# Kernel tuning notes

Measured on AMD Instinct MI355X. Metric: run time of the kernel, lower is better.

The kernel has to match this reference:

```python
import jax, jax.numpy as jnp
import numpy as np

# H36M parent-child joint pairs (the second assignment in the source overrides the first)
PARENT = np.array([[0,1],[1,2],[2,3],[0,4],[4,5],[5,6],[0,8],[8,14],[14,15],[15,16],[8,11],[11,12],[12,13],[8,10]])
NUM_JOINTS = 17
NUM_PAIRS = 14
GRID = 64


def create_heatmap(joint2d, size):
    # Gaussian with cov = 2*I evaluated on integer grid, normalized by its max.
    # Original: grid[i, j] = N([i, j]; mean=[x, y], 2I) / max -> pdf constant cancels.
    xy = joint2d * 64.0  # (B, J, 2)
    ii = jnp.arange(size, dtype=joint2d.dtype)
    dx = ii[None, None, :, None] - xy[..., 0][..., None, None]  # (B, J, size, 1)
    dy = ii[None, None, None, :] - xy[..., 1][..., None, None]  # (B, J, 1, size)
    d2 = dx * dx + dy * dy  # (B, J, size, size)
    g = jnp.exp(-d2 / 4.0)  # exp(-d2 / (2*var)), var = 2
    return g / jnp.max(g, axis=(2, 3), keepdims=True)


def setup_inputs() -> dict:
    key = jax.random.key(0)
    k1, k2, k3, k4 = jax.random.split(key, 4)
    B = 256
    return {
        "pred": jax.random.normal(k1, (B, NUM_JOINTS, 3), dtype=jnp.float32),
        "joints": jax.random.normal(k2, (B, NUM_JOINTS, 3), dtype=jnp.float32),
        "middle_out": jax.random.normal(k3, (B, NUM_JOINTS + 3 * NUM_PAIRS, GRID, GRID), dtype=jnp.float32),
        "joint2d": jax.random.uniform(k4, (B, NUM_JOINTS, 2), dtype=jnp.float32),
    }


def reference(pred, joints, middle_out, joint2d):
    eps = 0.1
    B, _, H, W = middle_out.shape
    # l3D: joints last dim == 3 branch
    l3d = jnp.mean(jnp.sum(jnp.abs(joints - pred[:, :NUM_JOINTS, :]), axis=(1, 2)))

    heatmap = create_heatmap(joint2d, H)  # (B, 17, 64, 64)

    # L2D: mean over batch of sum over joints of squared Frobenius norm (detached in original)
    diff = middle_out[:, :NUM_JOINTS] - heatmap
    L2D = jnp.mean(jnp.sum(jnp.sum(diff * diff, axis=(2, 3)), axis=1))

    # LHEM: vectorized heatmap triplets over batch and all 14 parent/child pairs
    p_idx = PARENT[:, 0]
    c_idx = PARENT[:, 1]
    hp = heatmap[:, p_idx]  # (B, 14, 64, 64)
    hc = heatmap[:, c_idx]  # (B, 14, 64, 64)
    d = joints[:, p_idx, 2] - joints[:, c_idx, 2]  # (B, 14)
    r = jnp.where(d > eps, 1, jnp.where(jnp.abs(d) < eps, 0, -1))[..., None, None]
    ch0 = jnp.where(r == -1, hc, 0.0)
    ch1 = jnp.where(r == 0, hp + hc, hp)
    ch2 = jnp.where(r == 1, hc, 0.0)
    T_GT = jnp.stack((ch0, ch1, ch2), axis=2)  # (B, 14, 3, 64, 64)
    T_pred = middle_out[:, NUM_JOINTS:NUM_JOINTS + 3 * NUM_PAIRS].reshape(B, NUM_PAIRS, 3, H, W)
    norms = jnp.sqrt(jnp.sum((T_GT - T_pred) ** 2, axis=(3, 4)))  # (B, 14, 3)
    LHEM = jnp.mean(jnp.sum(jnp.sum(norms, axis=2) ** 2, axis=1))

    Lint = 0.005 * (LHEM + L2D)
    # Original computes L2D / LHEM in detached numpy -> no gradient through Lint
    return l3d + jax.lax.stop_gradient(Lint)
```

## Files before the change

### kernel.cpp

```cpp
#include <hip/hip_runtime.h>
#include <math.h>

#define NJ 17
#define NP 14
#define NCH 59
#define BATCH 256
#define PSTRIDE 64

__constant__ int c_par0[NP] = {0, 1, 2, 0, 4, 5, 0, 8, 14, 15, 8, 11, 12, 8};
__constant__ int c_par1[NP] = {1, 2, 3, 4, 5, 6, 8, 14, 15, 16, 11, 12, 13, 10};

__device__ __forceinline__ float wave_reduce(float v) {
    #pragma unroll
    for (int off = 32; off; off >>= 1) v += __shfl_down(v, off, 64);
    return v;
}

__device__ __forceinline__ void heat_params(const float* __restrict__ joint2d,
                                            int b, int j,
                                            float& x, float& y, float& m) {
    x = joint2d[(b * NJ + j) * 2 + 0] * 64.f;
    y = joint2d[(b * NJ + j) * 2 + 1] * 64.f;
    const float rx = fminf(fmaxf(floorf(x + 0.5f), 0.f), 63.f);
    const float ry = fminf(fmaxf(floorf(y + 0.5f), 0.f), 63.f);
    m = (rx - x) * (rx - x) + (ry - y) * (ry - y);
}

__global__ __launch_bounds__(256) void slice_sum_kernel(
    const float* __restrict__ pred,
    const float* __restrict__ joints,
    const float* __restrict__ middle,
    const float* __restrict__ joint2d,
    float* __restrict__ partial)
{
    const int c   = blockIdx.x;
    const int b   = blockIdx.y;
    const int tid = threadIdx.x;

    const float4* __restrict__ src =
        (const float4*)(middle + ((size_t)b * NCH + c) * 4096);
    float4 r0 = src[tid];
    float4 r1 = src[tid + 256];
    float4 r2 = src[tid + 512];
    float4 r3 = src[tid + 768];

    float wp = 0.f, wc = 0.f;
    int jp = 0, jc = 0;
    if (c < NJ) {
        jp = c; wp = 1.f;
    } else {
        const int pi = c - NJ;
        const int p  = pi / 3;
        const int ch = pi - p * 3;
        jp = c_par0[p];
        jc = c_par1[p];
        const float dz = joints[(b * NJ + jp) * 3 + 2] - joints[(b * NJ + jc) * 3 + 2];
        const int rsign = (dz > 0.1f) ? 1 : ((fabsf(dz) < 0.1f) ? 0 : -1);
        if (ch == 0)      { wp = 0.f; wc = (rsign == -1) ? 1.f : 0.f; }
        else if (ch == 1) { wp = 1.f; wc = (rsign ==  0) ? 1.f : 0.f; }
        else              { wp = 0.f; wc = (rsign ==  1) ? 1.f : 0.f; }
    }

    float xp = 0.f, yp = 0.f, mp = 0.f;
    float xq = 0.f, yq = 0.f, mq = 0.f;
    if (wp != 0.f) heat_params(joint2d, b, jp, xp, yp, mp);
    if (wc != 0.f) heat_params(joint2d, b, jc, xq, yq, mq);

    const float col0 = (float)((4 * tid) & 63);
    const int   row0 = (4 * tid) >> 6;
    float cEp[4] = {0.f, 0.f, 0.f, 0.f};
    float cEc[4] = {0.f, 0.f, 0.f, 0.f};
    if (wp != 0.f) {
        #pragma unroll
        for (int q = 0; q < 4; ++q) {
            const float dy = (col0 + (float)q) - yp;
            cEp[q] = __expf(-0.25f * dy * dy);
        }
    }
    if (wc != 0.f) {
        #pragma unroll
        for (int q = 0; q < 4; ++q) {
            const float dy = (col0 + (float)q) - yq;
            cEc[q] = __expf(-0.25f * dy * dy);
        }
    }
    const float mp4 = 0.25f * mp;
    const float mq4 = 0.25f * mq;

    const float4 rr[4] = {r0, r1, r2, r3};
    float acc = 0.f;
    #pragma unroll
    for (int v = 0; v < 4; ++v) {
        const float fi = (float)(row0 + 16 * v);
        float rEp = 0.f, rEc = 0.f;
        if (wp != 0.f) {
            const float dx = fi - xp;
            rEp = __expf(fmaf(-0.25f * dx, dx, mp4));
        }
        if (wc != 0.f) {
            const float dx = fi - xq;
            rEc = __expf(fmaf(-0.25f * dx, dx, mq4));
        }
        const float mv[4] = {rr[v].x, rr[v].y, rr[v].z, rr[v].w};
        #pragma unroll
        for (int q = 0; q < 4; ++q) {
            const float tgt = fmaf(rEc, cEc[q], rEp * cEp[q]);
            const float d = tgt - mv[q];
            acc = fmaf(d, d, acc);
        }
    }

    acc = wave_reduce(acc);
    __shared__ float sred[4];
    if ((tid & 63) == 0) sred[tid >> 6] = acc;
    __syncthreads();
    if (tid == 0)
        partial[b * PSTRIDE + c] = sred[0] + sred[1] + sred[2] + sred[3];

    if (c == 0 && tid < 64) {
        float v = 0.f;
        if (tid < NJ * 3) {
            const int i = b * NJ * 3 + tid;
            v = fabsf(joints[i] - pred[i]);
        }
        v = wave_reduce(v);
        if (tid == 0) partial[b * PSTRIDE + 59] = v;
    }
}

__global__ __launch_bounds__(256) void finalize_kernel(
    const float* __restrict__ partial,
    float* __restrict__ out)
{
    const int b = threadIdx.x;
    const float4* __restrict__ row = (const float4*)(partial + b * PSTRIDE);
    float4 r[15];
    #pragma unroll
    for (int i = 0; i < 15; ++i) r[i] = row[i];
    const float* pr = (const float*)r;

    float l2d = 0.f;
    #pragma unroll
    for (int c = 0; c < NJ; ++c) l2d += pr[c];

    float hem = 0.f;
    #pragma unroll
    for (int p = 0; p < NP; ++p) {
        const float n = sqrtf(pr[NJ + 3 * p + 0]) +
                        sqrtf(pr[NJ + 3 * p + 1]) +
                        sqrtf(pr[NJ + 3 * p + 2]);
        hem = fmaf(n, n, hem);
    }

    double v = ((double)pr[59] + 0.005 * ((double)l2d + (double)hem)) * (1.0 / BATCH);

    #pragma unroll
    for (int off = 32; off; off >>= 1) v += __shfl_down(v, off, 64);
    __shared__ double sh[4];
    if ((b & 63) == 0) sh[b >> 6] = v;
    __syncthreads();
    if (b == 0) out[0] = (float)(sh[0] + sh[1] + sh[2] + sh[3]);
}

extern "C" void kernel_launch(void* const* d_in, const int* in_sizes, int n_in,
                              void* d_out, int out_size, void* d_ws, size_t ws_size,
                              hipStream_t stream) {
    const float* pred    = (const float*)d_in[0];
    const float* joints  = (const float*)d_in[1];
    const float* middle  = (const float*)d_in[2];
    const float* joint2d = (const float*)d_in[3];
    float* out  = (float*)d_out;
    float* part = (float*)d_ws;

    dim3 grid(NCH, BATCH);
    slice_sum_kernel<<<grid, 256, 0, stream>>>(pred, joints, middle, joint2d, part);
    finalize_kernel<<<1, 256, 0, stream>>>(part, out);
}
```

Before: 334.9 us.

## Assign one wavefront per channel slice and drop block-level reduction

Each 64-lane wavefront now processes one full 4096-element slice, loading 16 float4 values per lane. A block of 256 threads therefore covers four batch items, and the grid shrinks by four. This removes the shared-memory reduction and __syncthreads, and issues more loads in flight per thread. The cost is higher register use from the 16 float4s, which may lower occupancy, and the heatmap parameters now have to be computed per wavefront.

```diff
diff --git a/kernel.cpp b/kernel.cpp
--- a/kernel.cpp
+++ b/kernel.cpp
@@ -33,16 +33,15 @@
     const float* __restrict__ joint2d,
     float* __restrict__ partial)
 {
-    const int c   = blockIdx.x;
-    const int b   = blockIdx.y;
-    const int tid = threadIdx.x;
+    const int c    = blockIdx.x;
+    const int lane = threadIdx.x & 63;
+    const int b    = (blockIdx.y << 2) | (threadIdx.x >> 6);
 
     const float4* __restrict__ src =
-        (const float4*)(middle + ((size_t)b * NCH + c) * 4096);
-    float4 r0 = src[tid];
-    float4 r1 = src[tid + 256];
-    float4 r2 = src[tid + 512];
-    float4 r3 = src[tid + 768];
+        (const float4*)(middle + ((size_t)b * NCH + c) * 4096) + lane;
+    float4 d[16];
+    #pragma unroll
+    for (int j = 0; j < 16; ++j) d[j] = src[64 * j];
 
     float wp = 0.f, wc = 0.f;
     int jp = 0, jc = 0;
@@ -55,10 +54,10 @@
         jp = c_par0[p];
         jc = c_par1[p];
         const float dz = joints[(b * NJ + jp) * 3 + 2] - joints[(b * NJ + jc) * 3 + 2];
-        const int rsign = (dz > 0.1f) ? 1 : ((fabsf(dz) < 0.1f) ? 0 : -1);
-        if (ch == 0)      { wp = 0.f; wc = (rsign == -1) ? 1.f : 0.f; }
-        else if (ch == 1) { wp = 1.f; wc = (rsign ==  0) ? 1.f : 0.f; }
-        else              { wp = 0.f; wc = (rsign ==  1) ? 1.f : 0.f; }
+        const int rs = (dz > 0.1f) ? 1 : ((fabsf(dz) < 0.1f) ? 0 : -1);
+        if (ch == 0)      { wp = 0.f; wc = (rs == -1) ? 1.f : 0.f; }
+        else if (ch == 1) { wp = 1.f; wc = (rs ==  0) ? 1.f : 0.f; }
+        else              { wp = 0.f; wc = (rs ==  1) ? 1.f : 0.f; }
     }
 
     float xp = 0.f, yp = 0.f, mp = 0.f;
@@ -66,8 +65,8 @@
     if (wp != 0.f) heat_params(joint2d, b, jp, xp, yp, mp);
     if (wc != 0.f) heat_params(joint2d, b, jc, xq, yq, mq);
 
-    const float col0 = (float)((4 * tid) & 63);
-    const int   row0 = (4 * tid) >> 6;
+    const float col0 = (float)((4 * lane) & 63);
+    const float row0 = (float)(lane >> 4);
     float cEp[4] = {0.f, 0.f, 0.f, 0.f};
     float cEc[4] = {0.f, 0.f, 0.f, 0.f};
     if (wp != 0.f) {
@@ -87,11 +86,10 @@
     const float mp4 = 0.25f * mp;
     const float mq4 = 0.25f * mq;
 
-    const float4 rr[4] = {r0, r1, r2, r3};
     float acc = 0.f;
     #pragma unroll
-    for (int v = 0; v < 4; ++v) {
-        const float fi = (float)(row0 + 16 * v);
+    for (int j = 0; j < 16; ++j) {
+        const float fi = row0 + (float)(4 * j);
         float rEp = 0.f, rEc = 0.f;
         if (wp != 0.f) {
             const float dx = fi - xp;
@@ -101,30 +99,26 @@
             const float dx = fi - xq;
             rEc = __expf(fmaf(-0.25f * dx, dx, mq4));
         }
-        const float mv[4] = {rr[v].x, rr[v].y, rr[v].z, rr[v].w};
+        const float mv[4] = {d[j].x, d[j].y, d[j].z, d[j].w};
         #pragma unroll
         for (int q = 0; q < 4; ++q) {
             const float tgt = fmaf(rEc, cEc[q], rEp * cEp[q]);
-            const float d = tgt - mv[q];
-            acc = fmaf(d, d, acc);
+            const float df = tgt - mv[q];
+            acc = fmaf(df, df, acc);
         }
     }
 
     acc = wave_reduce(acc);
-    __shared__ float sred[4];
-    if ((tid & 63) == 0) sred[tid >> 6] = acc;
-    __syncthreads();
-    if (tid == 0)
-        partial[b * PSTRIDE + c] = sred[0] + sred[1] + sred[2] + sred[3];
+    if (lane == 0) partial[b * PSTRIDE + c] = acc;
 
-    if (c == 0 && tid < 64) {
+    if (c == 0) {
         float v = 0.f;
-        if (tid < NJ * 3) {
-            const int i = b * NJ * 3 + tid;
+        if (lane < NJ * 3) {
+            const int i = b * NJ * 3 + lane;
             v = fabsf(joints[i] - pred[i]);
         }
         v = wave_reduce(v);
-        if (tid == 0) partial[b * PSTRIDE + 59] = v;
+        if (lane == 0) partial[b * PSTRIDE + 59] = v;
     }
 }
 
@@ -172,7 +166,7 @@
     float* out  = (float*)d_out;
     float* part = (float*)d_ws;
 
-    dim3 grid(NCH, BATCH);
+    dim3 grid(NCH, BATCH / 4);
     slice_sum_kernel<<<grid, 256, 0, stream>>>(pred, joints, middle, joint2d, part);
     finalize_kernel<<<1, 256, 0, stream>>>(part, out);
 }
```

New measurement: 340.3 us. About the same (+1.6%).
